# Kernel tuning notes

Measured on AMD Instinct MI355X. Metric: run time of the kernel, lower is better.

## Reference

```python
import jax, jax.numpy as jnp
import numpy as np

HD, CD, BN = 128, 192, 16       # hidden_dim, context_dim, bin_num
OC = 2 * HD                     # ProjectionInputDepth out_chs
GC = HD + OC + CD               # GRU conv in-channels = hidden + (out_chs + context)
MAX_TREE_DEPTH = 6


def conv2d(x, w, b, ph, pw):
    y = jax.lax.conv_general_dilated(
        x, w, window_strides=(1, 1), padding=((ph, ph), (pw, pw)),
        dimension_numbers=('NCHW', 'OIHW', 'NCHW'))
    return y + b[None, :, None, None]


def setup_inputs():
    key = jax.random.key(0)
    B, H, W = 2, 120, 160
    ki = iter(jax.random.split(key, 20))
    def w(shape, s=0.05):
        return jax.random.normal(next(ki), shape, jnp.float32) * s
    z = lambda c: jnp.zeros((c,), jnp.float32)
    return {
        'depth': jax.random.uniform(next(ki), (B, 1, H, W), jnp.float32) * 80.0,
        'context': jax.random.normal(next(ki), (B, CD, H, W), jnp.float32),
        'gru_hidden': jax.random.normal(next(ki), (B, HD, H, W), jnp.float32),
        'encd1_w': w((HD, BN, 7, 7)), 'encd1_b': z(HD),
        'encd2_w': w((HD, HD, 3, 3)), 'encd2_b': z(HD),
        'encd3_w': w((HD, HD, 3, 3)), 'encd3_b': z(HD),
        'encd4_w': w((OC, HD, 3, 3)), 'encd4_b': z(OC),
        'convz1_w': w((HD, GC, 1, 5)), 'convz1_b': z(HD),
        'convr1_w': w((HD, GC, 1, 5)), 'convr1_b': z(HD),
        'convq1_w': w((HD, GC, 1, 5)), 'convq1_b': z(HD),
        'convz2_w': w((HD, GC, 5, 1)), 'convz2_b': z(HD),
        'convr2_w': w((HD, GC, 5, 1)), 'convr2_b': z(HD),
        'convq2_w': w((HD, GC, 5, 1)), 'convq2_b': z(HD),
        'ph1_w': w((HD, HD, 3, 3)), 'ph1_b': z(HD),
        'ph2_w': w((BN, HD, 3, 3)), 'ph2_b': z(BN),
        'bin_num': 16, 'min_depth': 0, 'max_depth': 80,
    }


def reference(depth, context, gru_hidden,
              encd1_w, encd1_b, encd2_w, encd2_b, encd3_w, encd3_b, encd4_w, encd4_b,
              convz1_w, convz1_b, convr1_w, convr1_b, convq1_w, convq1_b,
              convz2_w, convz2_b, convr2_w, convr2_b, convq2_w, convq2_b,
              ph1_w, ph1_b, ph2_w, ph2_b,
              bin_num, min_depth, max_depth):
    sg = jax.lax.stop_gradient
    B, _, H, W = depth.shape
    n = int(bin_num)
    mn, mx = float(min_depth), float(max_depth)
    # get_iebins: uniform bin edges via cumsum of constant intervals, (B, n+1, H, W)
    iv0 = jnp.concatenate([jnp.full((B, 1, H, W), mn, jnp.float32),
                           jnp.full((B, n, H, W), (mx - mn) / n, jnp.float32)], axis=1)
    bin_edges = jnp.cumsum(iv0, axis=1)
    current_depths = 0.5 * (bin_edges[:, :-1] + bin_edges[:, 1:])
    h = gru_hidden
    rs, cs, us = [], [], []
    for _ in range(MAX_TREE_DEPTH):
        cd = sg(current_depths)
        # ProjectionInputDepth
        d = jax.nn.relu(conv2d(cd, encd1_w, encd1_b, 3, 3))
        d = jax.nn.relu(conv2d(d, encd2_w, encd2_b, 1, 1))
        d = jax.nn.relu(conv2d(d, encd3_w, encd3_b, 1, 1))
        d = jax.nn.relu(conv2d(d, encd4_w, encd4_b, 1, 1))
        x = jnp.concatenate([d, context], axis=1)
        # SepConvGRU: horizontal (1,5) pass then vertical (5,1) pass
        hx = jnp.concatenate([h, x], axis=1)
        zg = jax.nn.sigmoid(conv2d(hx, convz1_w, convz1_b, 0, 2))
        rg = jax.nn.sigmoid(conv2d(hx, convr1_w, convr1_b, 0, 2))
        q = jnp.tanh(conv2d(jnp.concatenate([rg * h, x], axis=1), convq1_w, convq1_b, 0, 2))
        h = (1.0 - zg) * h + zg * q
        hx = jnp.concatenate([h, x], axis=1)
        zg = jax.nn.sigmoid(conv2d(hx, convz2_w, convz2_b, 2, 0))
        rg = jax.nn.sigmoid(conv2d(hx, convr2_w, convr2_b, 2, 0))
        q = jnp.tanh(conv2d(jnp.concatenate([rg * h, x], axis=1), convq2_w, convq2_b, 2, 0))
        h = (1.0 - zg) * h + zg * q
        # PHead -> per-bin probabilities
        prob = jax.nn.softmax(conv2d(jax.nn.relu(conv2d(h, ph1_w, ph1_b, 1, 1)), ph2_w, ph2_b, 1, 1), axis=1)
        depth_r = jnp.sum(prob * cd, axis=1, keepdims=True)        # (B,1,H,W)
        rs.append(depth_r)
        unc = jnp.sqrt(jnp.sum(prob * (cd - depth_r) ** 2, axis=1, keepdims=True))
        us.append(unc)
        # get_label: bin i with edges[i] <= d < edges[i+1]; 0 if out of range
        dv = sg(depth_r[:, 0])                                     # (B,H,W)
        cnt = jnp.sum((dv[:, None] >= bin_edges[:, 1:n]).astype(jnp.int32), axis=1)
        label = jnp.where(dv >= bin_edges[:, n], 0, cnt)[:, None]  # (B,1,H,W)
        cs.append(jnp.take_along_axis(cd, label, axis=1))
        # update_bins (mode 'direct', no grad): recenter on depth_r, width = uncertainty
        dr, um = sg(depth_r), sg(unc)
        start = jnp.maximum(dr - 0.5 * um, mn)
        ivals = jnp.concatenate([start, jnp.broadcast_to(um / n, (B, n, H, W))], axis=1)
        bin_edges = jnp.clip(jnp.cumsum(ivals, axis=1), mn, mx)
        current_depths = 0.5 * (bin_edges[:, :-1] + bin_edges[:, 1:])
    # stacked lists: (3, 6, B, 1, H, W) = [pred_depths_r, pred_depths_c, uncertainty_maps]
    return jnp.stack([jnp.stack(rs), jnp.stack(cs), jnp.stack(us)])
```

## Files before the change

### kernel.cpp

```cpp
#include <hip/hip_runtime.h>
#include <hip/hip_bf16.h>


#define HD  128
#define CDC 192
#define BN  16
#define OCH 256
#define GC  576
#define NB  2
#define HH  120
#define WW  160
#define HW  (HH*WW)
#define BHW (NB*HW)
#define PXT (BHW/128)
#define GXP (((PXT+7)/8)*8)
#define TPX (GXP/8)
#define PWW 168
#define PHH 126
#define PHW (PWW*PHH)
#define POFF(y,x) (((y)+3)*PWW + (x) + 4)

__device__ __forceinline__ float2 ldf2(const float* p){ return *(const float2*)p; }
__device__ __forceinline__ void stf2(float* p, float a, float b){
  *(float2*)p = make_float2(a,b);
}

typedef float f2 __attribute__((ext_vector_type(2), aligned(4)));
__device__ __forceinline__ f2 ldp(const float* p){ return *(const f2*)p; }

__device__ __forceinline__ void pkfma(f2& a, const f2 v, const float w){
  a = __builtin_elementwise_fma(v, f2{w, w}, a);
}

__global__ __launch_bounds__(256) void k_zero32(float* __restrict__ p, const size_t n){
  const size_t i = (size_t)blockIdx.x*256 + threadIdx.x;
  for (size_t k=i; k<n; k += (size_t)gridDim.x*256) p[k] = 0.f;
}
__global__ __launch_bounds__(256) void k_zero64(double* __restrict__ p, const size_t n){
  const size_t i = (size_t)blockIdx.x*256 + threadIdx.x;
  for (size_t k=i; k<n; k += (size_t)gridDim.x*256) p[k] = 0.0;
}

__global__ __launch_bounds__(256) void k_pad(const float* __restrict__ src,
        float* __restrict__ dst, const int nplanes){
  const int i = blockIdx.x*256 + threadIdx.x;
  if (i >= nplanes*HW) return;
  const int bc = i / HW, r = i - bc*HW;
  const int y = r / WW, x = r - y*WW;
  dst[(size_t)bc*PHW + POFF(y,x)] = src[i];
}

__global__ __launch_bounds__(256) void k_init(const float* __restrict__ gh,
        float* __restrict__ h, double* __restrict__ edges, double* __restrict__ cdp){
  const int i = blockIdx.x*256 + threadIdx.x;
  const int nh = NB*HD*HW;
  if (i < nh){
    const int bc = i / HW, r = i - bc*HW;
    const int y = r / WW, x = r - y*WW;
    h[(size_t)bc*PHW + POFF(y,x)] = gh[i];
  }
  if (i < BHW){
    const int b = i / HW, r = i - b*HW;
    const int y = r / WW, x = r - y*WW;
    const int pr = POFF(y,x);
    double e = 0.0;
    #pragma unroll
    for (int k=0;k<BN;++k){
      edges[(b*(BN+1)+k)*HW + r] = e;
      cdp[((size_t)b*BN+k)*PHW + pr] = e + 2.5;
      e += 5.0;
    }
    edges[(b*(BN+1)+BN)*HW + r] = e;
  }
}

__global__ __launch_bounds__(256) void k_wxpose(const float* __restrict__ w,
        float* __restrict__ wt, const int Cout, const int CIN, const int TAPS,
        const int n){
  const int i = blockIdx.x*256 + threadIdx.x;
  if (i >= n) return;
  const int ct = CIN*TAPS;
  const int o = i / ct;
  const int rem = i - o*ct;
  const int c = rem / TAPS;
  const int t = rem - c*TAPS;
  wt[((size_t)c*TAPS + t)*Cout + o] = w[i];
}

template<int GY>
__device__ __forceinline__ bool blk_decode(int& xs, int& yg){
  const int id  = blockIdx.x;
  const int xcd = id & 7;
  const int s   = id >> 3;
  yg = s & (GY-1);
  const int k = s / GY;
  xs = xcd*TPX + k;
  return xs < PXT;
}

__device__ __forceinline__ void pair_decode(const int xs, int& b, int& r0, int& po){
  const int lane = threadIdx.x & 63;
  const int pb = xs*128;
  b = pb / HW;
  r0 = pb - b*HW + 2*lane;
  const int y = r0 / WW, x = r0 - y*WW;
  po = POFF(y,x);
}

__global__ __launch_bounds__(256) void k_e1(const double* __restrict__ cdp,
        const float* __restrict__ wt, const float* __restrict__ bias,
        float* __restrict__ out){
  const int NACC = 8;
  int xs, yg;
  if (!blk_decode<4>(xs, yg)) return;
  const int wvu = __builtin_amdgcn_readfirstlane((int)(threadIdx.x >> 6));
  const int ow0 = (yg*4 + wvu)*NACC;
  int b, r0, po;
  pair_decode(xs, b, r0, po);
  double acc[2][NACC];
  #pragma unroll
  for (int j=0;j<NACC;++j){
    const double bj = (double)bias[ow0+j];
    acc[0][j]=bj; acc[1][j]=bj;
  }
  const double* inb = cdp + (size_t)b*16*PHW;
  #pragma unroll 1
  for (int t=0;t<49;++t){
    const int pot = po + (t/7 - 3)*PWW + (t%7 - 3);
    f2 ca[NACC];
    #pragma unroll
    for (int j=0;j<NACC;++j) ca[j] = f2{0.f, 0.f};
    const float* wr = wt + (size_t)t*HD + ow0;
    #pragma unroll 4
    for (int c=0;c<16;++c){
      const double* p = inb + (size_t)c*PHW + pot;
      const f2 v = {(float)p[0], (float)p[1]};
      #pragma unroll
      for (int j=0;j<NACC;++j) pkfma(ca[j], v, wr[j]);
      wr += (size_t)49*HD;
    }
    #pragma unroll
    for (int j=0;j<NACC;++j){ acc[0][j]+=(double)ca[j].x; acc[1][j]+=(double)ca[j].y; }
  }
  #pragma unroll
  for (int j=0;j<NACC;++j){
    double v0 = acc[0][j]; v0 = v0>0.0?v0:0.0;
    double v1 = acc[1][j]; v1 = v1>0.0?v1:0.0;
    stf2(out + ((size_t)b*HD + ow0 + j)*PHW + po, (float)v0, (float)v1);
  }
}

template<int NACC,int GY,int ACT>
__global__ __launch_bounds__(256) void k_fc3(const float* __restrict__ in,
        const float* __restrict__ wt, const float* __restrict__ bias,
        float* __restrict__ out, const int Cout){
  int xs, yg;
  if (!blk_decode<GY>(xs, yg)) return;
  const int wvu = __builtin_amdgcn_readfirstlane((int)(threadIdx.x >> 6));
  const int ow0 = (yg*4 + wvu)*NACC;
  int b, r0, po;
  pair_decode(xs, b, r0, po);
  double acc[2][NACC];
  #pragma unroll
  for (int j=0;j<NACC;++j){
    const double bj = (double)bias[ow0+j];
    acc[0][j]=bj; acc[1][j]=bj;
  }
  const float* inb = in + (size_t)b*128*PHW;
  #pragma unroll 1
  for (int t=0;t<9;++t){
    const int pot = po + (t/3 - 1)*PWW + (t%3 - 1);
    #pragma unroll 1
    for (int c0=0;c0<128;c0+=32){
      f2 ca[NACC];
      #pragma unroll
      for (int j=0;j<NACC;++j) ca[j] = f2{0.f, 0.f};
      const float* wr = wt + ((size_t)c0*9 + t)*Cout + ow0;
      #pragma unroll 8
      for (int c=0;c<32;++c){
        const f2 v = ldp(inb + (size_t)(c0+c)*PHW + pot);
        #pragma unroll
        for (int j=0;j<NACC;++j) pkfma(ca[j], v, wr[j]);
        wr += (size_t)9*Cout;
      }
      #pragma unroll
      for (int j=0;j<NACC;++j){ acc[0][j]+=(double)ca[j].x; acc[1][j]+=(double)ca[j].y; }
    }
  }
  #pragma unroll
  for (int j=0;j<NACC;++j){
    double v0 = acc[0][j], v1 = acc[1][j];
    if (ACT==1){ v0 = v0>0.0?v0:0.0; v1 = v1>0.0?v1:0.0; }
    stf2(out + ((size_t)b*Cout + ow0 + j)*PHW + po, (float)v0, (float)v1);
  }
}

template<int C,int NACC>
__device__ __forceinline__ void seg2(const float* __restrict__ plane, const int pot,
    const float* __restrict__ wz0, const float* __restrict__ wr0,
    double az[2][NACC], double ar[2][NACC]){
  #pragma unroll 1
  for (int c0=0;c0<C;c0+=32){
    f2 cz[NACC], cr[NACC];
    #pragma unroll
    for (int j=0;j<NACC;++j){ cz[j]=f2{0.f,0.f}; cr[j]=f2{0.f,0.f}; }
    const float* wz = wz0 + (size_t)c0*5*HD;
    const float* wr = wr0 + (size_t)c0*5*HD;
    #pragma unroll 4
    for (int c=0;c<32;++c){
      const f2 v = ldp(plane + (size_t)(c0+c)*PHW + pot);
      #pragma unroll
      for (int j=0;j<NACC;++j){
        pkfma(cz[j], v, wz[j]);
        pkfma(cr[j], v, wr[j]);
      }
      wz += 5*HD; wr += 5*HD;
    }
    #pragma unroll
    for (int j=0;j<NACC;++j){
      az[0][j]+=(double)cz[j].x; az[1][j]+=(double)cz[j].y;
      ar[0][j]+=(double)cr[j].x; ar[1][j]+=(double)cr[j].y;
    }
  }
}
template<int C,int NACC>
__device__ __forceinline__ void seg3(const float* __restrict__ plane, const int pot,
    const float* __restrict__ wz0, const float* __restrict__ wr0,
    const float* __restrict__ wq0,
    double az[2][NACC], double ar[2][NACC], double aq[2][NACC]){
  #pragma unroll 1
  for (int c0=0;c0<C;c0+=32){
    f2 cz[NACC], cr[NACC], cq[NACC];
    #pragma unroll
    for (int j=0;j<NACC;++j){ cz[j]=f2{0.f,0.f}; cr[j]=f2{0.f,0.f}; cq[j]=f2{0.f,0.f}; }
    const float* wz = wz0 + (size_t)c0*5*HD;
    const float* wr = wr0 + (size_t)c0*5*HD;
    const float* wq = wq0 + (size_t)c0*5*HD;
    #pragma unroll 4
    for (int c=0;c<32;++c){
      const f2 v = ldp(plane + (size_t)(c0+c)*PHW + pot);
      #pragma unroll
      for (int j=0;j<NACC;++j){
        pkfma(cz[j], v, wz[j]);
        pkfma(cr[j], v, wr[j]);
        pkfma(cq[j], v, wq[j]);
      }
      wz += 5*HD; wr += 5*HD; wq += 5*HD;
    }
    #pragma unroll
    for (int j=0;j<NACC;++j){
      az[0][j]+=(double)cz[j].x; az[1][j]+=(double)cz[j].y;
      ar[0][j]+=(double)cr[j].x; ar[1][j]+=(double)cr[j].y;
      aq[0][j]+=(double)cq[j].x; aq[1][j]+=(double)cq[j].y;
    }
  }
}
template<int C,int NACC>
__device__ __forceinline__ void seg1(const float* __restrict__ plane, const int pot,
    const float* __restrict__ wq0, double aq[2][NACC]){
  #pragma unroll 1
  for (int c0=0;c0<C;c0+=32){
    f2 cq[NACC];
    #pragma unroll
    for (int j=0;j<NACC;++j) cq[j]=f2{0.f,0.f};
    const float* wq = wq0 + (size_t)c0*5*HD;
    #pragma unroll 8
    for (int c=0;c<32;++c){
      const f2 v = ldp(plane + (size_t)(c0+c)*PHW + pot);
      #pragma unroll
      for (int j=0;j<NACC;++j) pkfma(cq[j], v, wq[j]);
      wq += 5*HD;
    }
    #pragma unroll
    for (int j=0;j<NACC;++j){ aq[0][j]+=(double)cq[j].x; aq[1][j]+=(double)cq[j].y; }
  }
}

template<int VERT>
__global__ __launch_bounds__(256) void k_zrx(
    const float* __restrict__ h, const float* __restrict__ d4,
    const float* __restrict__ ctxp,
    const float* __restrict__ wtz, const float* __restrict__ wtr,
    const float* __restrict__ wtq,
    const float* __restrict__ bz, const float* __restrict__ br,
    const float* __restrict__ bq,
    float* __restrict__ zg, float* __restrict__ rgh, float* __restrict__ qx){
  const int NACC = 4;
  int xs, yg;
  if (!blk_decode<8>(xs, yg)) return;
  const int wvu = __builtin_amdgcn_readfirstlane((int)(threadIdx.x >> 6));
  const int ow0 = (yg*4 + wvu)*NACC;
  int b, r0, po;
  pair_decode(xs, b, r0, po);
  double az[2][NACC], ar[2][NACC], aq[2][NACC];
  #pragma unroll
  for (int j=0;j<NACC;++j){
    const double bzj=(double)bz[ow0+j], brj=(double)br[ow0+j], bqj=(double)bq[ow0+j];
    az[0][j]=bzj; az[1][j]=bzj; ar[0][j]=brj; ar[1][j]=brj; aq[0][j]=bqj; aq[1][j]=bqj;
  }
  const float* hb = h   + (size_t)b*HD *PHW;
  const float* db = d4  + (size_t)b*OCH*PHW;
  const float* cb = ctxp+ (size_t)b*CDC*PHW;
  #pragma unroll 1
  for (int t=0;t<5;++t){
    const int pot = po + (VERT ? (t-2)*PWW : (t-2));
    seg2<HD ,NACC>(hb, pot, wtz + (size_t)t*HD + ow0,
                            wtr + (size_t)t*HD + ow0, az, ar);
    seg3<OCH,NACC>(db, pot, wtz + ((size_t)HD*5 + t)*HD + ow0,
                            wtr + ((size_t)HD*5 + t)*HD + ow0,
                            wtq + ((size_t)HD*5 + t)*HD + ow0, az, ar, aq);
    seg3<CDC,NACC>(cb, pot, wtz + ((size_t)(HD+OCH)*5 + t)*HD + ow0,
                            wtr + ((size_t)(HD+OCH)*5 + t)*HD + ow0,
                            wtq + ((size_t)(HD+OCH)*5 + t)*HD + ow0, az, ar, aq);
  }
  #pragma unroll
  for (int j=0;j<NACC;++j){
    const size_t pp = ((size_t)b*HD + ow0 + j)*PHW + po;
    const float2 hv = ldf2(h + pp);
    const double z0 = 1.0/(1.0+exp(-az[0][j])), z1 = 1.0/(1.0+exp(-az[1][j]));
    const double g0 = (1.0/(1.0+exp(-ar[0][j]))) * (double)hv.x;
    const double g1 = (1.0/(1.0+exp(-ar[1][j]))) * (double)hv.y;
    stf2(zg  + pp, (float)z0, (float)z1);
    stf2(rgh + pp, (float)g0, (float)g1);
    stf2(qx + ((size_t)b*HD + ow0 + j)*HW + r0, (float)aq[0][j], (float)aq[1][j]);
  }
}

template<int VERT>
__global__ __launch_bounds__(256) void k_qh(
    const float* __restrict__ rgh, const float* __restrict__ wtq,
    const float* __restrict__ qx, const float* __restrict__ zg,
    float* __restrict__ h){
  const int NACC = 8;
  int xs, yg;
  if (!blk_decode<4>(xs, yg)) return;
  const int wvu = __builtin_amdgcn_readfirstlane((int)(threadIdx.x >> 6));
  const int ow0 = (yg*4 + wvu)*NACC;
  int b, r0, po;
  pair_decode(xs, b, r0, po);
  double aq[2][NACC];
  #pragma unroll
  for (int j=0;j<NACC;++j){
    const float2 q0 = ldf2(qx + ((size_t)b*HD + ow0 + j)*HW + r0);
    aq[0][j] = (double)q0.x; aq[1][j] = (double)q0.y;
  }
  const float* gb = rgh + (size_t)b*HD*PHW;
  #pragma unroll 1
  for (int t=0;t<5;++t){
    const int pot = po + (VERT ? (t-2)*PWW : (t-2));
    seg1<HD,NACC>(gb, pot, wtq + (size_t)t*HD + ow0, aq);
  }
  #pragma unroll
  for (int j=0;j<NACC;++j){
    const size_t pp = ((size_t)b*HD + ow0 + j)*PHW + po;
    const float2 zv = ldf2(zg + pp);
    const float2 hv = ldf2(h  + pp);
    const double z0=(double)zv.x, z1=(double)zv.y;
    const double n0 = (1.0-z0)*(double)hv.x + z0*tanh(aq[0][j]);
    const double n1 = (1.0-z1)*(double)hv.y + z1*tanh(aq[1][j]);
    stf2(h + pp, (float)n0, (float)n1);
  }
}

__global__ __launch_bounds__(256) void k_stats(const float* __restrict__ lg,
    double* __restrict__ edges, double* __restrict__ cdp, float* __restrict__ out,
    const int it){
  const int px = blockIdx.x*256 + threadIdx.x;
  const int b = px / HW, r = px - b*HW;
  const int y = r / WW, x = r - y*WW;
  const int pr = POFF(y,x);
  double l[BN], p[BN], c[BN];
  double m = -1e300;
  #pragma unroll
  for (int k=0;k<BN;++k){ l[k] = (double)lg[((size_t)b*BN+k)*PHW + pr]; m = l[k]>m?l[k]:m; }
  double s = 0.0;
  #pragma unroll
  for (int k=0;k<BN;++k){ p[k] = exp(l[k]-m); s += p[k]; }
  double dr = 0.0;
  #pragma unroll
  for (int k=0;k<BN;++k){ c[k] = cdp[((size_t)b*BN+k)*PHW + pr]; p[k] = p[k]/s; dr += p[k]*c[k]; }
  double var = 0.0;
  #pragma unroll
  for (int k=0;k<BN;++k){ const double d = c[k]-dr; var += p[k]*(d*d); }
  const double un = sqrt(var);
  int cnt = 0;
  #pragma unroll
  for (int k=1;k<BN;++k) cnt += (dr >= edges[(b*(BN+1)+k)*HW + r]) ? 1 : 0;
  const double etop = edges[(b*(BN+1)+BN)*HW + r];
  const int label = (dr >= etop) ? 0 : cnt;
  double csv = c[0];
  #pragma unroll
  for (int k=1;k<BN;++k) csv = (label==k) ? c[k] : csv;
  out[((0*6+it)*NB + b)*HW + r] = (float)dr;
  out[((1*6+it)*NB + b)*HW + r] = (float)csv;
  out[((2*6+it)*NB + b)*HW + r] = (float)un;
  const double start = dr - 0.5*un > 0.0 ? dr - 0.5*un : 0.0;
  const double step = un * (1.0/BN);
  double e = start;
  double prev = e < 0.0 ? 0.0 : (e > 80.0 ? 80.0 : e);
  edges[(b*(BN+1)+0)*HW + r] = prev;
  #pragma unroll
  for (int k=1;k<=BN;++k){
    e = e + step;
    const double ec = e < 0.0 ? 0.0 : (e > 80.0 ? 80.0 : e);
    edges[(b*(BN+1)+k)*HW + r] = ec;
    cdp[((size_t)b*BN + (k-1))*PHW + pr] = 0.5*(prev + ec);
    prev = ec;
  }
}

extern "C" void kernel_launch(void* const* d_in, const int* in_sizes, int n_in,
                              void* d_out, int out_size, void* d_ws, size_t ws_size,
                              hipStream_t stream){
  const float* ctx = (const float*)d_in[1];
  const float* gh  = (const float*)d_in[2];
  const float *e1w=(const float*)d_in[3],  *e1b=(const float*)d_in[4];
  const float *e2w=(const float*)d_in[5],  *e2b=(const float*)d_in[6];
  const float *e3w=(const float*)d_in[7],  *e3b=(const float*)d_in[8];
  const float *e4w=(const float*)d_in[9],  *e4b=(const float*)d_in[10];
  const float *z1w=(const float*)d_in[11], *z1b=(const float*)d_in[12];
  const float *r1w=(const float*)d_in[13], *r1b=(const float*)d_in[14];
  const float *q1w=(const float*)d_in[15], *q1b=(const float*)d_in[16];
  const float *z2w=(const float*)d_in[17], *z2b=(const float*)d_in[18];
  const float *r2w=(const float*)d_in[19], *r2b=(const float*)d_in[20];
  const float *q2w=(const float*)d_in[21], *q2b=(const float*)d_in[22];
  const float *p1w=(const float*)d_in[23], *p1b=(const float*)d_in[24];
  const float *p2w=(const float*)d_in[25], *p2b=(const float*)d_in[26];
  float* out = (float*)d_out;

  double* edges = (double*)d_ws;
  double* cdp   = edges + (size_t)NB*(BN+1)*HW;
  float* fb    = (float*)(cdp + (size_t)NB*BN*PHW);
  float* hp    = fb;
  float* d4p   = hp    + (size_t)NB*HD *PHW;
  float* bufAp = d4p   + (size_t)NB*OCH*PHW;
  float* bufBp = bufAp + (size_t)NB*HD *PHW;
  float* ctxp  = bufBp + (size_t)NB*HD *PHW;
  float* lgtsp = ctxp  + (size_t)NB*CDC*PHW;
  const size_t npad32 = (size_t)NB*(HD+OCH+HD+HD+CDC+BN)*PHW;
  float* qx   = lgtsp + (size_t)NB*BN*PHW;
  float* wp   = qx + (size_t)NB*HD*HW;
  float* we1 = wp;              wp += (size_t)HD*16*49;
  float* we2 = wp;              wp += (size_t)HD*HD*9;
  float* we3 = wp;              wp += (size_t)HD*HD*9;
  float* we4 = wp;              wp += (size_t)OCH*HD*9;
  float* wz1 = wp;              wp += (size_t)HD*GC*5;
  float* wr1 = wp;              wp += (size_t)HD*GC*5;
  float* wq1 = wp;              wp += (size_t)HD*GC*5;
  float* wz2 = wp;              wp += (size_t)HD*GC*5;
  float* wr2 = wp;              wp += (size_t)HD*GC*5;
  float* wq2 = wp;              wp += (size_t)HD*GC*5;
  float* wp1 = wp;              wp += (size_t)HD*HD*9;
  float* wp2 = wp;              wp += (size_t)16*HD*9;

  const dim3 blk(256);

  k_zero32<<<dim3(2048), blk, 0, stream>>>(fb, npad32);
  k_zero64<<<dim3(1024), blk, 0, stream>>>(cdp, (size_t)NB*BN*PHW);

  #define XP(src,dst,Cout_,CIN_,TAPS_) { const int n=(Cout_)*(CIN_)*(TAPS_); \
    k_wxpose<<<dim3((n+255)/256), blk, 0, stream>>>(src, dst, Cout_, CIN_, TAPS_, n); }
  XP(e1w, we1, HD, 16, 49); XP(e2w, we2, HD, HD, 9); XP(e3w, we3, HD, HD, 9);
  XP(e4w, we4, OCH, HD, 9);
  XP(z1w, wz1, HD, GC, 5); XP(r1w, wr1, HD, GC, 5); XP(q1w, wq1, HD, GC, 5);
  XP(z2w, wz2, HD, GC, 5); XP(r2w, wr2, HD, GC, 5); XP(q2w, wq2, HD, GC, 5);
  XP(p1w, wp1, HD, HD, 9); XP(p2w, wp2, 16, HD, 9);
  #undef XP

  k_pad<<<dim3((NB*CDC*HW+255)/256), blk, 0, stream>>>(ctx, ctxp, NB*CDC);
  k_init<<<dim3((NB*HD*HW+255)/256), blk, 0, stream>>>(gh, hp, edges, cdp);

  const int G8 = GXP*8, G4 = GXP*4, G1 = GXP;
  const int PXB = BHW/256;

  for (int it=0; it<6; ++it){
    k_e1        <<<dim3(G4), blk, 0, stream>>>(cdp,   we1, e1b, bufAp);
    k_fc3<8,4,1><<<dim3(G4), blk, 0, stream>>>(bufAp, we2, e2b, bufBp, HD);
    k_fc3<8,4,1><<<dim3(G4), blk, 0, stream>>>(bufBp, we3, e3b, bufAp, HD);
    k_fc3<8,8,1><<<dim3(G8), blk, 0, stream>>>(bufAp, we4, e4b, d4p,  OCH);
    k_zrx<0><<<dim3(G8), blk, 0, stream>>>(hp, d4p, ctxp, wz1, wr1, wq1,
                                           z1b, r1b, q1b, bufAp, bufBp, qx);
    k_qh <0><<<dim3(G4), blk, 0, stream>>>(bufBp, wq1, qx, bufAp, hp);
    k_zrx<1><<<dim3(G8), blk, 0, stream>>>(hp, d4p, ctxp, wz2, wr2, wq2,
                                           z2b, r2b, q2b, bufAp, bufBp, qx);
    k_qh <1><<<dim3(G4), blk, 0, stream>>>(bufBp, wq2, qx, bufAp, hp);
    k_fc3<8,4,1><<<dim3(G4), blk, 0, stream>>>(hp,    wp1, p1b, bufAp, HD);
    k_fc3<4,1,0><<<dim3(G1), blk, 0, stream>>>(bufAp, wp2, p2b, lgtsp, 16);
    k_stats<<<dim3(PXB), blk, 0, stream>>>(lgtsp, edges, cdp, out, it);
  }
}
```

Baseline: 25.53 ms.

## Stage input channel tiles in LDS for 3x3 and GRU convolution kernels

The 3x3 conv and the GRU z/r/q kernels now load each 32-channel slice of input pixels into shared memory once per block, with __syncthreads around the copy. The four waves then read from LDS instead of each issuing its own global loads. The goal is to cut redundant global and L2 traffic, since every wave of a block covers the same pixels for different output channels. The cost is two barriers per channel chunk and extra LDS traffic, with no double buffering to overlap the loads with compute.

```diff
diff --git a/kernel.cpp b/kernel.cpp
--- a/kernel.cpp
+++ b/kernel.cpp
@@ -19,6 +19,8 @@
 #define PHH 126
 #define PHW (PWW*PHH)
 #define POFF(y,x) (((y)+3)*PWW + (x) + 4)
+#define LDSW 144
+#define LDSF2 (LDSW/2)
 
 __device__ __forceinline__ float2 ldf2(const float* p){ return *(const float2*)p; }
 __device__ __forceinline__ void stf2(float* p, float a, float b){
@@ -30,6 +32,18 @@
 
 __device__ __forceinline__ void pkfma(f2& a, const f2 v, const float w){
   a = __builtin_elementwise_fma(v, f2{w, w}, a);
+}
+
+__device__ __forceinline__ void stage32(const float* __restrict__ plane,
+        const int c0, const int gbase, float* __restrict__ sm){
+  const int tid = threadIdx.x;
+  #pragma unroll
+  for (int k=0;k<9;++k){
+    const int idx = tid + k*256;
+    const int c = idx / LDSF2, o = idx - c*LDSF2;
+    const f2 v = ldp(plane + (size_t)(c0+c)*PHW + gbase + 2*o);
+    *(f2*)&sm[c*LDSW + 2*o] = v;
+  }
 }
 
 __global__ __launch_bounds__(256) void k_zero32(float* __restrict__ p, const size_t n){
@@ -98,11 +112,15 @@
   return xs < PXT;
 }
 
-__device__ __forceinline__ void pair_decode(const int xs, int& b, int& r0, int& po){
+__device__ __forceinline__ void pair_decode(const int xs, int& b, int& r0,
+                                            int& po, int& po0){
   const int lane = threadIdx.x & 63;
   const int pb = xs*128;
   b = pb / HW;
-  r0 = pb - b*HW + 2*lane;
+  const int rb = pb - b*HW;
+  const int y0 = rb / WW, x0 = rb - y0*WW;
+  po0 = POFF(y0,x0);
+  r0 = rb + 2*lane;
   const int y = r0 / WW, x = r0 - y*WW;
   po = POFF(y,x);
 }
@@ -115,8 +133,8 @@
   if (!blk_decode<4>(xs, yg)) return;
   const int wvu = __builtin_amdgcn_readfirstlane((int)(threadIdx.x >> 6));
   const int ow0 = (yg*4 + wvu)*NACC;
-  int b, r0, po;
-  pair_decode(xs, b, r0, po);
+  int b, r0, po, po0;
+  pair_decode(xs, b, r0, po, po0);
   double acc[2][NACC];
   #pragma unroll
   for (int j=0;j<NACC;++j){
@@ -150,16 +168,102 @@
   }
 }
 
+template<int NACC>
+__device__ __forceinline__ void segfc(const float* __restrict__ sm, const int loff,
+    const float* __restrict__ wr, const size_t wstride, double acc[2][NACC]){
+  f2 ca[NACC];
+  #pragma unroll
+  for (int j=0;j<NACC;++j) ca[j] = f2{0.f, 0.f};
+  #pragma unroll 8
+  for (int c=0;c<32;++c){
+    const float* row = sm + c*LDSW + loff;
+    f2 v; v.x = row[0]; v.y = row[1];
+    #pragma unroll
+    for (int j=0;j<NACC;++j) pkfma(ca[j], v, wr[j]);
+    wr += wstride;
+  }
+  #pragma unroll
+  for (int j=0;j<NACC;++j){ acc[0][j]+=(double)ca[j].x; acc[1][j]+=(double)ca[j].y; }
+}
+
+template<int NACC>
+__device__ __forceinline__ void seg2c(const float* __restrict__ sm, const int loff,
+    const float* __restrict__ wz, const float* __restrict__ wr,
+    double az[2][NACC], double ar[2][NACC]){
+  f2 cz[NACC], cr[NACC];
+  #pragma unroll
+  for (int j=0;j<NACC;++j){ cz[j]=f2{0.f,0.f}; cr[j]=f2{0.f,0.f}; }
+  #pragma unroll 4
+  for (int c=0;c<32;++c){
+    const float* row = sm + c*LDSW + loff;
+    f2 v; v.x = row[0]; v.y = row[1];
+    #pragma unroll
+    for (int j=0;j<NACC;++j){ pkfma(cz[j], v, wz[j]); pkfma(cr[j], v, wr[j]); }
+    wz += 5*HD; wr += 5*HD;
+  }
+  #pragma unroll
+  for (int j=0;j<NACC;++j){
+    az[0][j]+=(double)cz[j].x; az[1][j]+=(double)cz[j].y;
+    ar[0][j]+=(double)cr[j].x; ar[1][j]+=(double)cr[j].y;
+  }
+}
+
+template<int NACC>
+__device__ __forceinline__ void seg3c(const float* __restrict__ sm, const int loff,
+    const float* __restrict__ wz, const float* __restrict__ wr,
+    const float* __restrict__ wq,
+    double az[2][NACC], double ar[2][NACC], double aq[2][NACC]){
+  f2 cz[NACC], cr[NACC], cq[NACC];
+  #pragma unroll
+  for (int j=0;j<NACC;++j){ cz[j]=f2{0.f,0.f}; cr[j]=f2{0.f,0.f}; cq[j]=f2{0.f,0.f}; }
+  #pragma unroll 4
+  for (int c=0;c<32;++c){
+    const float* row = sm + c*LDSW + loff;
+    f2 v; v.x = row[0]; v.y = row[1];
+    #pragma unroll
+    for (int j=0;j<NACC;++j){
+      pkfma(cz[j], v, wz[j]); pkfma(cr[j], v, wr[j]); pkfma(cq[j], v, wq[j]);
+    }
+    wz += 5*HD; wr += 5*HD; wq += 5*HD;
+  }
+  #pragma unroll
+  for (int j=0;j<NACC;++j){
+    az[0][j]+=(double)cz[j].x; az[1][j]+=(double)cz[j].y;
+    ar[0][j]+=(double)cr[j].x; ar[1][j]+=(double)cr[j].y;
+    aq[0][j]+=(double)cq[j].x; aq[1][j]+=(double)cq[j].y;
+  }
+}
+
+template<int NACC>
+__device__ __forceinline__ void seg1c(const float* __restrict__ sm, const int loff,
+    const float* __restrict__ wq, double aq[2][NACC]){
+  f2 cq[NACC];
+  #pragma unroll
+  for (int j=0;j<NACC;++j) cq[j]=f2{0.f,0.f};
+  #pragma unroll 8
+  for (int c=0;c<32;++c){
+    const float* row = sm + c*LDSW + loff;
+    f2 v; v.x = row[0]; v.y = row[1];
+    #pragma unroll
+    for (int j=0;j<NACC;++j) pkfma(cq[j], v, wq[j]);
+    wq += 5*HD;
+  }
+  #pragma unroll
+  for (int j=0;j<NACC;++j){ aq[0][j]+=(double)cq[j].x; aq[1][j]+=(double)cq[j].y; }
+}
+
 template<int NACC,int GY,int ACT>
 __global__ __launch_bounds__(256) void k_fc3(const float* __restrict__ in,
         const float* __restrict__ wt, const float* __restrict__ bias,
         float* __restrict__ out, const int Cout){
+  __shared__ float sm[32*LDSW];
   int xs, yg;
   if (!blk_decode<GY>(xs, yg)) return;
   const int wvu = __builtin_amdgcn_readfirstlane((int)(threadIdx.x >> 6));
   const int ow0 = (yg*4 + wvu)*NACC;
-  int b, r0, po;
-  pair_decode(xs, b, r0, po);
+  int b, r0, po, po0;
+  pair_decode(xs, b, r0, po, po0);
+  const int loff = po - po0 + 2;
   double acc[2][NACC];
   #pragma unroll
   for (int j=0;j<NACC;++j){
@@ -169,22 +273,14 @@
   const float* inb = in + (size_t)b*128*PHW;
   #pragma unroll 1
   for (int t=0;t<9;++t){
-    const int pot = po + (t/3 - 1)*PWW + (t%3 - 1);
+    const int gb = po0 - 2 + (t/3 - 1)*PWW + (t%3 - 1);
     #pragma unroll 1
     for (int c0=0;c0<128;c0+=32){
-      f2 ca[NACC];
-      #pragma unroll
-      for (int j=0;j<NACC;++j) ca[j] = f2{0.f, 0.f};
-      const float* wr = wt + ((size_t)c0*9 + t)*Cout + ow0;
-      #pragma unroll 8
-      for (int c=0;c<32;++c){
-        const f2 v = ldp(inb + (size_t)(c0+c)*PHW + pot);
-        #pragma unroll
-        for (int j=0;j<NACC;++j) pkfma(ca[j], v, wr[j]);
-        wr += (size_t)9*Cout;
-      }
-      #pragma unroll
-      for (int j=0;j<NACC;++j){ acc[0][j]+=(double)ca[j].x; acc[1][j]+=(double)ca[j].y; }
+      __syncthreads();
+      stage32(inb, c0, gb, sm);
+      __syncthreads();
+      segfc<NACC>(sm, loff, wt + ((size_t)c0*9 + t)*Cout + ow0,
+                  (size_t)9*Cout, acc);
     }
   }
   #pragma unroll
@@ -192,87 +288,6 @@
     double v0 = acc[0][j], v1 = acc[1][j];
     if (ACT==1){ v0 = v0>0.0?v0:0.0; v1 = v1>0.0?v1:0.0; }
     stf2(out + ((size_t)b*Cout + ow0 + j)*PHW + po, (float)v0, (float)v1);
-  }
-}
-
-template<int C,int NACC>
-__device__ __forceinline__ void seg2(const float* __restrict__ plane, const int pot,
-    const float* __restrict__ wz0, const float* __restrict__ wr0,
-    double az[2][NACC], double ar[2][NACC]){
-  #pragma unroll 1
-  for (int c0=0;c0<C;c0+=32){
-    f2 cz[NACC], cr[NACC];
-    #pragma unroll
-    for (int j=0;j<NACC;++j){ cz[j]=f2{0.f,0.f}; cr[j]=f2{0.f,0.f}; }
-    const float* wz = wz0 + (size_t)c0*5*HD;
-    const float* wr = wr0 + (size_t)c0*5*HD;
-    #pragma unroll 4
-    for (int c=0;c<32;++c){
-      const f2 v = ldp(plane + (size_t)(c0+c)*PHW + pot);
-      #pragma unroll
-      for (int j=0;j<NACC;++j){
-        pkfma(cz[j], v, wz[j]);
-        pkfma(cr[j], v, wr[j]);
-      }
-      wz += 5*HD; wr += 5*HD;
-    }
-    #pragma unroll
-    for (int j=0;j<NACC;++j){
-      az[0][j]+=(double)cz[j].x; az[1][j]+=(double)cz[j].y;
-      ar[0][j]+=(double)cr[j].x; ar[1][j]+=(double)cr[j].y;
-    }
-  }
-}
-template<int C,int NACC>
-__device__ __forceinline__ void seg3(const float* __restrict__ plane, const int pot,
-    const float* __restrict__ wz0, const float* __restrict__ wr0,
-    const float* __restrict__ wq0,
-    double az[2][NACC], double ar[2][NACC], double aq[2][NACC]){
-  #pragma unroll 1
-  for (int c0=0;c0<C;c0+=32){
-    f2 cz[NACC], cr[NACC], cq[NACC];
-    #pragma unroll
-    for (int j=0;j<NACC;++j){ cz[j]=f2{0.f,0.f}; cr[j]=f2{0.f,0.f}; cq[j]=f2{0.f,0.f}; }
-    const float* wz = wz0 + (size_t)c0*5*HD;
-    const float* wr = wr0 + (size_t)c0*5*HD;
-    const float* wq = wq0 + (size_t)c0*5*HD;
-    #pragma unroll 4
-    for (int c=0;c<32;++c){
-      const f2 v = ldp(plane + (size_t)(c0+c)*PHW + pot);
-      #pragma unroll
-      for (int j=0;j<NACC;++j){
-        pkfma(cz[j], v, wz[j]);
-        pkfma(cr[j], v, wr[j]);
-        pkfma(cq[j], v, wq[j]);
-      }
-      wz += 5*HD; wr += 5*HD; wq += 5*HD;
-    }
-    #pragma unroll
-    for (int j=0;j<NACC;++j){
-      az[0][j]+=(double)cz[j].x; az[1][j]+=(double)cz[j].y;
-      ar[0][j]+=(double)cr[j].x; ar[1][j]+=(double)cr[j].y;
-      aq[0][j]+=(double)cq[j].x; aq[1][j]+=(double)cq[j].y;
-    }
-  }
-}
-template<int C,int NACC>
-__device__ __forceinline__ void seg1(const float* __restrict__ plane, const int pot,
-    const float* __restrict__ wq0, double aq[2][NACC]){
-  #pragma unroll 1
-  for (int c0=0;c0<C;c0+=32){
-    f2 cq[NACC];
-    #pragma unroll
-    for (int j=0;j<NACC;++j) cq[j]=f2{0.f,0.f};
-    const float* wq = wq0 + (size_t)c0*5*HD;
-    #pragma unroll 8
-    for (int c=0;c<32;++c){
-      const f2 v = ldp(plane + (size_t)(c0+c)*PHW + pot);
-      #pragma unroll
-      for (int j=0;j<NACC;++j) pkfma(cq[j], v, wq[j]);
-      wq += 5*HD;
-    }
-    #pragma unroll
-    for (int j=0;j<NACC;++j){ aq[0][j]+=(double)cq[j].x; aq[1][j]+=(double)cq[j].y; }
   }
 }
 
@@ -286,12 +301,14 @@
     const float* __restrict__ bq,
     float* __restrict__ zg, float* __restrict__ rgh, float* __restrict__ qx){
   const int NACC = 4;
+  __shared__ float sm[32*LDSW];
   int xs, yg;
   if (!blk_decode<8>(xs, yg)) return;
   const int wvu = __builtin_amdgcn_readfirstlane((int)(threadIdx.x >> 6));
   const int ow0 = (yg*4 + wvu)*NACC;
-  int b, r0, po;
-  pair_decode(xs, b, r0, po);
+  int b, r0, po, po0;
+  pair_decode(xs, b, r0, po, po0);
+  const int loff = po - po0 + 2;
   double az[2][NACC], ar[2][NACC], aq[2][NACC];
   #pragma unroll
   for (int j=0;j<NACC;++j){
@@ -303,15 +320,37 @@
   const float* cb = ctxp+ (size_t)b*CDC*PHW;
   #pragma unroll 1
   for (int t=0;t<5;++t){
-    const int pot = po + (VERT ? (t-2)*PWW : (t-2));
-    seg2<HD ,NACC>(hb, pot, wtz + (size_t)t*HD + ow0,
-                            wtr + (size_t)t*HD + ow0, az, ar);
-    seg3<OCH,NACC>(db, pot, wtz + ((size_t)HD*5 + t)*HD + ow0,
-                            wtr + ((size_t)HD*5 + t)*HD + ow0,
-                            wtq + ((size_t)HD*5 + t)*HD + ow0, az, ar, aq);
-    seg3<CDC,NACC>(cb, pot, wtz + ((size_t)(HD+OCH)*5 + t)*HD + ow0,
-                            wtr + ((size_t)(HD+OCH)*5 + t)*HD + ow0,
-                            wtq + ((size_t)(HD+OCH)*5 + t)*HD + ow0, az, ar, aq);
+    const int gb = po0 - 2 + (VERT ? (t-2)*PWW : (t-2));
+    #pragma unroll 1
+    for (int c0=0;c0<HD;c0+=32){
+      __syncthreads();
+      stage32(hb, c0, gb, sm);
+      __syncthreads();
+      seg2c<NACC>(sm, loff, wtz + (size_t)t*HD + ow0 + (size_t)c0*5*HD,
+                            wtr + (size_t)t*HD + ow0 + (size_t)c0*5*HD, az, ar);
+    }
+    #pragma unroll 1
+    for (int c0=0;c0<OCH;c0+=32){
+      __syncthreads();
+      stage32(db, c0, gb, sm);
+      __syncthreads();
+      seg3c<NACC>(sm, loff,
+                  wtz + ((size_t)HD*5 + t)*HD + ow0 + (size_t)c0*5*HD,
+                  wtr + ((size_t)HD*5 + t)*HD + ow0 + (size_t)c0*5*HD,
+                  wtq + ((size_t)HD*5 + t)*HD + ow0 + (size_t)c0*5*HD,
+                  az, ar, aq);
+    }
+    #pragma unroll 1
+    for (int c0=0;c0<CDC;c0+=32){
+      __syncthreads();
+      stage32(cb, c0, gb, sm);
+      __syncthreads();
+      seg3c<NACC>(sm, loff,
+                  wtz + ((size_t)(HD+OCH)*5 + t)*HD + ow0 + (size_t)c0*5*HD,
+                  wtr + ((size_t)(HD+OCH)*5 + t)*HD + ow0 + (size_t)c0*5*HD,
+                  wtq + ((size_t)(HD+OCH)*5 + t)*HD + ow0 + (size_t)c0*5*HD,
+                  az, ar, aq);
+    }
   }
   #pragma unroll
   for (int j=0;j<NACC;++j){
@@ -332,23 +371,31 @@
     const float* __restrict__ qx, const float* __restrict__ zg,
     float* __restrict__ h){
   const int NACC = 8;
+  __shared__ float sm[32*LDSW];
   int xs, yg;
   if (!blk_decode<4>(xs, yg)) return;
   const int wvu = __builtin_amdgcn_readfirstlane((int)(threadIdx.x >> 6));
   const int ow0 = (yg*4 + wvu)*NACC;
-  int b, r0, po;
-  pair_decode(xs, b, r0, po);
+  int b, r0, po, po0;
+  pair_decode(xs, b, r0, po, po0);
+  const int loff = po - po0 + 2;
   double aq[2][NACC];
   #pragma unroll
   for (int j=0;j<NACC;++j){
     const float2 q0 = ldf2(qx + ((size_t)b*HD + ow0 + j)*HW + r0);
     aq[0][j] = (double)q0.x; aq[1][j] = (double)q0.y;
   }
-  const float* gb = rgh + (size_t)b*HD*PHW;
+  const float* gb_ = rgh + (size_t)b*HD*PHW;
   #pragma unroll 1
   for (int t=0;t<5;++t){
-    const int pot = po + (VERT ? (t-2)*PWW : (t-2));
-    seg1<HD,NACC>(gb, pot, wtq + (size_t)t*HD + ow0, aq);
+    const int gb = po0 - 2 + (VERT ? (t-2)*PWW : (t-2));
+    #pragma unroll 1
+    for (int c0=0;c0<HD;c0+=32){
+      __syncthreads();
+      stage32(gb_, c0, gb, sm);
+      __syncthreads();
+      seg1c<NACC>(sm, loff, wtq + (size_t)t*HD + ow0 + (size_t)c0*5*HD, aq);
+    }
   }
   #pragma unroll
   for (int j=0;j<NACC;++j){
```

Measured after the change: 42.66 ms. +67.1%, slower.
